# Kernel tuning notes

Hardware: AMD Instinct MI355X
Metric: run time of the kernel (lower is better)

## Reference

```python
import jax, jax.numpy as jnp
import numpy as np
import math

K = 1.0          # Lorentz curvature parameter (points satisfy -t^2 + |s|^2 = -K)
SQRT_K = 1.0
HEADS = 8
HEAD_DIM = 64
EPS_LN = 1e-5


def add_time(xs):
    # lift space vector onto the hyperboloid: t = sqrt(|s|^2 + K)
    t = jnp.sqrt(jnp.sum(xs * xs, axis=-1, keepdims=True) + K)
    return jnp.concatenate([t, xs], axis=-1)


def logmap0(x):
    t, s = x[..., :1], x[..., 1:]
    d = SQRT_K * jnp.arccosh(jnp.maximum(t / SQRT_K, 1.0))
    sn = jnp.maximum(jnp.linalg.norm(s, axis=-1, keepdims=True), 1e-8)
    return jnp.concatenate([jnp.zeros_like(t), d * s / sn], axis=-1)


def expmap0(u):
    s = u[..., 1:]
    n = jnp.maximum(jnp.linalg.norm(s, axis=-1, keepdims=True), 1e-8)
    t = SQRT_K * jnp.cosh(n / SQRT_K)
    return jnp.concatenate([t, SQRT_K * jnp.sinh(n / SQRT_K) * s / n], axis=-1)


def lorentz_ln(x, g, b):
    # LayerNorm on space coords, then recompute time
    s = x[..., 1:]
    mu = jnp.mean(s, axis=-1, keepdims=True)
    var = jnp.var(s, axis=-1, keepdims=True)
    s = (s - mu) / jnp.sqrt(var + EPS_LN) * g + b
    return add_time(s)


def lfc(x, W, activation=None):
    # LorentzFullyConnected: linear on full input -> space coords, recompute time
    s = x @ W.T
    if activation is not None:
        s = activation(s)
    return add_time(s)


def lfc_heads(x, W):
    b, n, _ = x.shape
    s = (x @ W.T).reshape(b, n, HEADS, HEAD_DIM).transpose(0, 2, 1, 3)
    return add_time(s)  # (b, h, n, head_dim+1), per-head time coordinate


def _mha_haa(x, Wq, Wk, Wv, Wo, temperature, beta_raw, tau_raw, lambda_raw):
    q = lfc_heads(x, Wq)
    k = lfc_heads(x, Wk)
    v = lfc_heads(x, Wv)
    q_t, k_t = q[..., :1], k[..., :1]
    q_s, k_s = q[..., 1:], k[..., 1:]
    # Lorentz inner product <q,k>_L = -t_q t_k + <s_q, s_k>, shape (b,h,n,n)
    inner_QK = -q_t @ jnp.swapaxes(k_t, -1, -2) + q_s @ jnp.swapaxes(k_s, -1, -2)
    inner_OQ = -SQRT_K * q_t                       # (b,h,n,1)
    inner_OK = -SQRT_K * jnp.swapaxes(k_t, -1, -2)  # (b,h,1,n)
    norm_sq_QK = jnp.maximum(inner_QK ** 2 / K - K, 0.0)
    norm_sq_OQ = jnp.maximum(inner_OQ ** 2 / K - K, 0.0)
    numer_Z = inner_OK + inner_QK * inner_OQ / K
    denom_Z = jnp.sqrt(norm_sq_QK * norm_sq_OQ + 0.005 ** 2)
    Z = jnp.clip(numer_Z / denom_Z, -1.0, 1.0)
    c_tilde = jnp.arccosh(jnp.maximum(q_t / SQRT_K, 1.0 + 0.001))
    beta = jax.nn.softplus(beta_raw)
    B = jnp.sqrt(jax.nn.relu(1.0 - (beta / jnp.sinh(c_tilde)) ** 2) + 1e-8)
    lam = jax.nn.softplus(lambda_raw)
    dist_raw = SQRT_K * jnp.arccosh(jnp.maximum(-inner_QK / K, 1.0 + 0.001))
    d_soft = 40.0 * jnp.tanh(dist_raw / 40.0)
    sd = d_soft / 15.0
    H = sd + jax.nn.softplus(-2.0 * sd) - math.log(2.0)
    tau = jax.nn.softplus(tau_raw)
    m = 0.1
    Phi = jax.nn.softplus(B + Z - m) - math.log(1.0 + math.exp(-m))
    score = jax.nn.softmax((-lam * H - tau * Phi) / temperature, axis=-1)
    # Lorentz expmap aggregation: weighted mean in tangent space at origin
    v_tan = logmap0(v)
    mean_tan = (score @ v_tan) / (jnp.sum(score, axis=-1, keepdims=True) + 1e-8)
    attn = expmap0(mean_tan).transpose(0, 2, 1, 3)  # (b,n,h,head_dim+1)
    b_, n_ = attn.shape[:2]
    a_s = attn[..., 1:].reshape(b_, n_, -1)   # (b,n,h*head_dim)
    a_t = attn[..., :1].reshape(b_, n_, -1)   # (b,n,h)
    t2 = jnp.sum(a_t ** 2, axis=-1, keepdims=True) - (HEADS - 1) * K
    attn = jnp.concatenate([jnp.sqrt(jnp.maximum(t2, 1e-8)), a_s], axis=-1)
    return lfc(attn, Wo)


def reference(x, Wq, Wk, Wv, Wo, W1, W2, ln1_g, ln1_b, ln2_g, ln2_b,
              temperature, beta_raw, tau_raw, lambda_raw):
    out = _mha_haa(lorentz_ln(x, ln1_g, ln1_b), Wq, Wk, Wv, Wo,
                   temperature, beta_raw, tau_raw, lambda_raw)
    out_s = out[..., 1:] + x[..., 1:]                 # residual on space coords
    y = lorentz_ln(add_time(out_s), ln2_g, ln2_b)
    h = lfc(y, W1, activation=lambda z: jax.nn.gelu(z, approximate=False))
    h = lfc(h, W2)
    out_s = h[..., 1:] + out_s
    return add_time(out_s)


def setup_inputs() -> dict:
    key = jax.random.key(0)
    ks = jax.random.split(key, 8)
    B, N, D = 2, 1024, 513
    xs = 0.5 * jax.random.normal(ks[0], (B, N, D - 1), dtype=jnp.float32)
    x = add_time(xs)
    sc = 1.0 / math.sqrt(D)
    return {
        "x": x,
        "Wq": sc * jax.random.normal(ks[1], (512, 513), dtype=jnp.float32),
        "Wk": sc * jax.random.normal(ks[2], (512, 513), dtype=jnp.float32),
        "Wv": sc * jax.random.normal(ks[3], (512, 513), dtype=jnp.float32),
        "Wo": sc * jax.random.normal(ks[4], (512, 513), dtype=jnp.float32),
        "W1": sc * jax.random.normal(ks[5], (2048, 513), dtype=jnp.float32),
        "W2": (1.0 / math.sqrt(2049)) * jax.random.normal(ks[6], (512, 2049), dtype=jnp.float32),
        "ln1_g": jnp.ones((512,), jnp.float32),
        "ln1_b": jnp.zeros((512,), jnp.float32),
        "ln2_g": jnp.ones((512,), jnp.float32),
        "ln2_b": jnp.zeros((512,), jnp.float32),
        "temperature": jnp.ones((1,), jnp.float32),
        "beta_raw": jnp.full((1,), math.log(math.e - 1.0), jnp.float32),
        "tau_raw": jnp.full((1,), math.log(math.exp(0.1) - 1.0), jnp.float32),
        "lambda_raw": jnp.full((1,), math.log(math.e - 1.0), jnp.float32),
    }
```

## Files before the change

kernel.cpp:

```cpp
#include <hip/hip_runtime.h>
#include <math.h>

#define DEV static __device__ __forceinline__

typedef __bf16 bf16_t;
typedef __bf16 bf16x8 __attribute__((ext_vector_type(8)));
typedef float f32x4 __attribute__((ext_vector_type(4)));

#define MFMA16(a,b,c) __builtin_amdgcn_mfma_f32_16x16x32_bf16(a,b,c,0,0,0)

DEV float frcp(float x){ return __builtin_amdgcn_rcpf(x); }
DEV float softplus_fast(float x){
  return fmaxf(x, 0.f) + __logf(1.f + __expf(-fabsf(x)));
}
DEV float tanh_fast(float z){
  float e2 = __expf(2.f * z);
  return (e2 - 1.f) * frcp(e2 + 1.f);
}
DEV float gelu_fast(float v){
  float u = 0.7978845608028654f * fmaf(0.044715f * v, v * v, v);
  u = fminf(fmaxf(u, -15.f), 15.f);
  return 0.5f * v * (1.f + tanh_fast(u));
}

DEV void gl_lds16(const void* g, void* l) {
  __builtin_amdgcn_global_load_lds((const __attribute__((address_space(1))) void*)g,
                                   (__attribute__((address_space(3))) void*)l, 16, 0, 0);
}

DEV float waveReduceSum(float v){
  #pragma unroll
  for (int o = 32; o > 0; o >>= 1) v += __shfl_xor(v, o, 64);
  return v;
}
DEV float blockReduceSum(float v, float* sh){
  v = waveReduceSum(v);
  int w = threadIdx.x >> 6;
  int nw = blockDim.x >> 6;
  __syncthreads();
  if ((threadIdx.x & 63) == 0) sh[w] = v;
  __syncthreads();
  float r = sh[0];
  for (int i = 1; i < nw; i++) r += sh[i];
  return r;
}

__global__ __launch_bounds__(256) void conv_all(
    const float* __restrict__ Wq, const float* __restrict__ Wk,
    const float* __restrict__ Wv, const float* __restrict__ Wo,
    const float* __restrict__ W1, const float* __restrict__ W2,
    bf16_t* __restrict__ Wqkvb, bf16_t* __restrict__ Wob,
    bf16_t* __restrict__ W1b, bf16_t* __restrict__ W2b,
    float* __restrict__ wqkv0, float* __restrict__ wo0,
    float* __restrict__ w10, float* __restrict__ w20)
{
  long i = (long)blockIdx.x * 256 + threadIdx.x;
  if (i < 786432) {
    long r = i >> 9; int c = (int)(i & 511);
    const float* src = (r < 512) ? Wq + r * 513 : (r < 1024) ? Wk + (r - 512) * 513 : Wv + (r - 1024) * 513;
    Wqkvb[i] = (bf16_t)src[c + 1];
  } else if (i < 1048576) {
    long j = i - 786432;
    long r = j >> 9; int c = (int)(j & 511);
    Wob[j] = (bf16_t)Wo[r * 513 + c + 1];
  } else if (i < 2097152) {
    long j = i - 1048576;
    long r = j >> 9; int c = (int)(j & 511);
    W1b[j] = (bf16_t)W1[r * 513 + c + 1];
  } else if (i < 3145728) {
    long j = i - 2097152;
    long r = j >> 11; int c = (int)(j & 2047);
    W2b[j] = (bf16_t)W2[r * 2049 + c + 1];
  } else if (i < 3150336) {
    int j = (int)(i - 3145728);
    if (j < 1536) {
      wqkv0[j] = (j < 512) ? Wq[(long)j * 513] : (j < 1024) ? Wk[(long)(j - 512) * 513] : Wv[(long)(j - 1024) * 513];
    } else if (j < 2048) wo0[j - 1536] = Wo[(long)(j - 1536) * 513];
    else if (j < 4096)  w10[j - 2048] = W1[(long)(j - 2048) * 513];
    else                w20[j - 4096] = W2[(long)(j - 4096) * 2049];
  }
}

__global__ __launch_bounds__(256) void ln_fwd(
    const float* __restrict__ xin,
    const float* __restrict__ g, const float* __restrict__ b,
    bf16_t* __restrict__ y, float* __restrict__ ty)
{
  __shared__ float sh[8];
  int row = blockIdx.x;
  const float* xr = xin + (long)row * 513 + 1;
  int t = threadIdx.x;
  float a0 = xr[t], a1 = xr[t + 256];
  float s  = blockReduceSum(a0 + a1, sh);
  float s2 = blockReduceSum(a0 * a0 + a1 * a1, sh);
  float mu = s * (1.f / 512.f);
  float var = s2 * (1.f / 512.f) - mu * mu;
  float inv = rsqrtf(var + 1e-5f);
  float y0 = (a0 - mu) * inv * g[t] + b[t];
  float y1v = (a1 - mu) * inv * g[t + 256] + b[t + 256];
  float q = blockReduceSum(y0 * y0 + y1v * y1v, sh);
  bf16_t* yr = y + (long)row * 512;
  yr[t] = (bf16_t)y0;
  yr[t + 256] = (bf16_t)y1v;
  if (t == 0) ty[row] = sqrtf(q + 1.f);
}

__global__ __launch_bounds__(256) void res_ln(
    const float* __restrict__ woA, const float* __restrict__ woB,
    const float* __restrict__ ch2, const float* __restrict__ wo0,
    const float* __restrict__ xin,
    const float* __restrict__ g, const float* __restrict__ b,
    float* __restrict__ outs,
    bf16_t* __restrict__ y, float* __restrict__ ty)
{
  __shared__ float sh[8];
  int row = blockIdx.x;
  int t = threadIdx.x;
  const float* c = ch2 + (long)row * 8;
  float cs = ((c[0] + c[1]) + (c[2] + c[3])) + ((c[4] + c[5]) + (c[6] + c[7]));
  float tattn = sqrtf(fmaxf(cs - 7.f, 1e-8f));
  long i0 = (long)row * 512 + t, i1 = i0 + 256;
  float a0 = woA[i0] + woB[i0] + tattn * wo0[t]       + xin[(long)row * 513 + 1 + t];
  float a1 = woA[i1] + woB[i1] + tattn * wo0[t + 256] + xin[(long)row * 513 + 1 + t + 256];
  outs[i0] = a0;
  outs[i1] = a1;
  float s  = blockReduceSum(a0 + a1, sh);
  float s2 = blockReduceSum(a0 * a0 + a1 * a1, sh);
  float mu = s * (1.f / 512.f);
  float var = s2 * (1.f / 512.f) - mu * mu;
  float inv = rsqrtf(var + 1e-5f);
  float y0 = (a0 - mu) * inv * g[t] + b[t];
  float y1v = (a1 - mu) * inv * g[t + 256] + b[t + 256];
  float q = blockReduceSum(y0 * y0 + y1v * y1v, sh);
  bf16_t* yr = y + (long)row * 512;
  yr[t] = (bf16_t)y0;
  yr[t + 256] = (bf16_t)y1v;
  if (t == 0) ty[row] = sqrtf(q + 1.f);
}

__global__ __launch_bounds__(256) void final_k(
    const float* __restrict__ h2A, const float* __restrict__ h2B,
    const bf16_t* __restrict__ hb, const float* __restrict__ w20,
    const float* __restrict__ outs,
    float* __restrict__ out)
{
  __shared__ float sh[8];
  int row = blockIdx.x;
  int t = threadIdx.x;
  bf16x8 hv = *(const bf16x8*)&hb[(long)row * 2048 + t * 8];
  float ss = 0.f;
  #pragma unroll
  for (int j = 0; j < 8; j++) { float f = (float)hv[j]; ss = fmaf(f, f, ss); }
  float th = sqrtf(blockReduceSum(ss, sh) + 1.f);
  long i0 = (long)row * 512 + t, i1 = i0 + 256;
  float o0 = h2A[i0] + h2B[i0] + th * w20[t]       + outs[i0];
  float o1 = h2A[i1] + h2B[i1] + th * w20[t + 256] + outs[i1];
  float q = blockReduceSum(o0 * o0 + o1 * o1, sh);
  float* yr = out + (long)row * 513;
  yr[1 + t] = o0;
  yr[1 + t + 256] = o1;
  if (t == 0) yr[0] = sqrtf(q + 1.f);
}

__global__ __launch_bounds__(256) void qkv_prep(
    const bf16_t* __restrict__ qkvsb,
    float* __restrict__ qt, float* __restrict__ kt, float* __restrict__ Bi,
    bf16_t* __restrict__ VTt,
    const float* __restrict__ beta_p)
{
  __shared__ bf16_t tile[64 * 72];
  int z = blockIdx.y, b = z >> 3, h = z & 7;
  int n0 = blockIdx.x * 64;
  int t = threadIdx.x;
  int r = t >> 2, c4 = t & 3;
  long rowbase = (long)(b * 1024 + n0 + r) * 1536 + h * 64 + c4 * 16;
  bf16x8 q0 = *(const bf16x8*)(qkvsb + rowbase);
  bf16x8 q1 = *(const bf16x8*)(qkvsb + rowbase + 8);
  bf16x8 k0 = *(const bf16x8*)(qkvsb + rowbase + 512);
  bf16x8 k1 = *(const bf16x8*)(qkvsb + rowbase + 520);
  bf16x8 v0 = *(const bf16x8*)(qkvsb + rowbase + 1024);
  bf16x8 v1 = *(const bf16x8*)(qkvsb + rowbase + 1032);
  float q2 = 0.f, k2 = 0.f, vv2 = 0.f;
  #pragma unroll
  for (int e = 0; e < 8; e++) {
    float a0 = (float)q0[e], a1 = (float)q1[e];
    float b0 = (float)k0[e], b1 = (float)k1[e];
    float c0 = (float)v0[e], c1 = (float)v1[e];
    q2 = fmaf(a0, a0, fmaf(a1, a1, q2));
    k2 = fmaf(b0, b0, fmaf(b1, b1, k2));
    vv2 = fmaf(c0, c0, fmaf(c1, c1, vv2));
  }
  q2 += __shfl_xor(q2, 1, 64); q2 += __shfl_xor(q2, 2, 64);
  k2 += __shfl_xor(k2, 1, 64); k2 += __shfl_xor(k2, 2, 64);
  vv2 += __shfl_xor(vv2, 1, 64); vv2 += __shfl_xor(vv2, 2, 64);
  float vT = sqrtf(1.f + vv2);
  float sn0 = sqrtf(vv2);
  float coef = __logf(vT + sn0) * frcp(fmaxf(sn0, 1e-8f));
  if (c4 == 0) {
    int ob = z * 1024 + n0 + r;
    float qT = sqrtf(1.f + q2);
    qt[ob] = qT;
    kt[ob] = sqrtf(1.f + k2);
    float beta = softplus_fast(beta_p[0]);
    float xq = fmaxf(qT, 1.001f);
    float sh_ = sqrtf(fmaxf(xq * xq - 1.f, 0.f));
    float rr = beta * frcp(sh_);
    Bi[ob] = sqrtf(fmaxf(1.f - rr * rr, 0.f) + 1e-8f);
  }
  #pragma unroll
  for (int e = 0; e < 8; e++) {
    tile[(c4 * 16 + e) * 72 + r]     = (bf16_t)(coef * (float)v0[e]);
    tile[(c4 * 16 + 8 + e) * 72 + r] = (bf16_t)(coef * (float)v1[e]);
  }
  __syncthreads();
  int d = t >> 2, cc = (t & 3) * 16;
  bf16x8 o0 = *(const bf16x8*)&tile[d * 72 + cc];
  bf16x8 o1 = *(const bf16x8*)&tile[d * 72 + cc + 8];
  bf16_t* dst = VTt + (long)z * 64 * 1024 + (long)d * 1024 + n0 + cc;
  *(bf16x8*)dst = o0;
  *(bf16x8*)(dst + 8) = o1;
}

__global__ __launch_bounds__(256) void attn_fused(
    const bf16_t* __restrict__ qkvsb,
    const bf16_t* __restrict__ VTt,
    const float* __restrict__ qt, const float* __restrict__ kt,
    const float* __restrict__ Bi,
    bf16_t* __restrict__ attnb,
    float* __restrict__ ch2,
    const float* __restrict__ lam_p, const float* __restrict__ tau_p,
    const float* __restrict__ temp_p)
{
  __shared__ bf16_t Ks[64 * 64];
  __shared__ bf16_t Vs[64 * 64];
  __shared__ bf16_t Ps[32 * 72];
  __shared__ float ot[32 * 65];
  __shared__ float sh_qt[32], sh_Bc[32], sh_kt[64], rs[32];

  const int t = threadIdx.x;
  const int w = t >> 6;
  const int lane = t & 63;
  const int lm = lane & 15, lh = lane >> 4;
  const int z = blockIdx.y, b = z >> 3, h = z & 7;
  const int n0 = blockIdx.x * 32;
  const int sb = (((lane & 7) ^ (lane >> 3)) << 4);
  const int r8 = lane >> 3;

  float lam = softplus_fast(lam_p[0]);
  float tau = softplus_fast(tau_p[0]);
  float invT = frcp(temp_p[0]);
  float A1 = -lam * invT, A2 = -tau * invT;
  float A2h = 0.5f * A2, K0 = A2 * 0.048750465f;

  if (t < 32) {
    sh_qt[t] = qt[z * 1024 + n0 + t];
    sh_Bc[t] = Bi[z * 1024 + n0 + t] - 0.1f;
    rs[t] = 0.f;
  }

  const bf16_t* qbase = qkvsb + ((long)(b * 1024 + n0) * 1536 + h * 64);
  gl_lds16((const char*)(qbase + (long)(w * 8 + r8) * 1536) + sb, (char*)Ks + w * 1024);
  __syncthreads();
  bf16x8 qf[2][2];
  #pragma unroll
  for (int i = 0; i < 2; i++)
    #pragma unroll
    for (int kk = 0; kk < 2; kk++)
      qf[i][kk] = *(const bf16x8*)&Ks[(i * 16 + lm) * 64 + (((kk * 4 + lh) ^ (lm & 7)) << 3)];

  f32x4 oacc[2] = {};
  float racc[2][4] = {};

  const bf16_t* kbase = qkvsb + ((long)b * 1024 * 1536 + 512 + h * 64);
  const bf16_t* vbase = VTt + (long)z * 64 * 1024;
  const int sl0 = ((lh) ^ (lm & 7)) << 3;
  const int sl1 = ((4 + lh) ^ (lm & 7)) << 3;

  for (int kv = 0; kv < 16; kv++) {
    __syncthreads();
    {
      const bf16_t* kb = kbase + (long)(kv * 64) * 1536;
      gl_lds16((const char*)(kb + (long)(w * 16 + r8) * 1536) + sb,     (char*)Ks + (w * 2) * 1024);
      gl_lds16((const char*)(kb + (long)(w * 16 + 8 + r8) * 1536) + sb, (char*)Ks + (w * 2 + 1) * 1024);
      const bf16_t* vb = vbase + kv * 64;
      gl_lds16((const char*)(vb + (long)(w * 16 + r8) * 1024) + sb,     (char*)Vs + (w * 2) * 1024);
      gl_lds16((const char*)(vb + (long)(w * 16 + 8 + r8) * 1024) + sb, (char*)Vs + (w * 2 + 1) * 1024);
    }
    if (t < 64) sh_kt[t] = kt[z * 1024 + kv * 64 + t];
    __syncthreads();

    f32x4 sacc[2] = {};
    bf16x8 kf0 = *(const bf16x8*)&Ks[(w * 16 + lm) * 64 + sl0];
    bf16x8 kf1 = *(const bf16x8*)&Ks[(w * 16 + lm) * 64 + sl1];
    sacc[0] = MFMA16(qf[0][0], kf0, sacc[0]);
    sacc[0] = MFMA16(qf[0][1], kf1, sacc[0]);
    sacc[1] = MFMA16(qf[1][0], kf0, sacc[1]);
    sacc[1] = MFMA16(qf[1][1], kf1, sacc[1]);

    float ktv = sh_kt[w * 16 + lm];
    #pragma unroll
    for (int i = 0; i < 2; i++) {
      #pragma unroll
      for (int q = 0; q < 4; q++) {
        int r = i * 16 + lh * 4 + q;
        float qtv = sh_qt[r], Bc = sh_Bc[r];
        float nOQ = fmaf(qtv, qtv, -1.f);
        float inner = fmaf(-qtv, ktv, sacc[i][q]);
        float nQK = fmaxf(fmaf(inner, inner, -1.f), 0.f);
        float ri = __builtin_amdgcn_rsqf(fmaf(nQK, nOQ, 2.5e-5f));
        float zr = fmaf(inner, qtv, ktv) * ri;
        float Zc = fminf(fmaxf(-zr, -1.f), 1.f);
        float xx = fmaxf(-inner, 1.001f);
        float u = fmaf(__log2f(xx), 0.01732868f, 0.01732868f);
        float p = fminf(u * u, 0.09f);
        float H = p * fmaf(p, -6.584f, 3.5556f);
        float a = Zc + Bc;
        float a2 = a * a;
        float lc = a2 * fmaf(a2, fmaf(a2, 0.00034722f, -0.0052083f), 0.125f);
        float lgt = fmaf(A1, H, fmaf(A2, lc, fmaf(A2h, a, K0)));
        float e = __expf(lgt);
        Ps[r * 72 + w * 16 + lm] = (bf16_t)e;
        racc[i][q] += e;
      }
    }
    __syncthreads();

    bf16x8 va0 = *(const bf16x8*)&Vs[(w * 16 + lm) * 64 + sl0];
    bf16x8 va1 = *(const bf16x8*)&Vs[(w * 16 + lm) * 64 + sl1];
    bf16x8 pb00 = *(const bf16x8*)&Ps[lm * 72 + lh * 8];
    bf16x8 pb01 = *(const bf16x8*)&Ps[lm * 72 + 32 + lh * 8];
    bf16x8 pb10 = *(const bf16x8*)&Ps[(16 + lm) * 72 + lh * 8];
    bf16x8 pb11 = *(const bf16x8*)&Ps[(16 + lm) * 72 + 32 + lh * 8];
    oacc[0] = MFMA16(va0, pb00, oacc[0]);
    oacc[0] = MFMA16(va1, pb01, oacc[0]);
    oacc[1] = MFMA16(va0, pb10, oacc[1]);
    oacc[1] = MFMA16(va1, pb11, oacc[1]);
  }

  #pragma unroll
  for (int i = 0; i < 2; i++)
    #pragma unroll
    for (int q = 0; q < 4; q++) {
      float v = racc[i][q];
      v += __shfl_xor(v, 1, 64);
      v += __shfl_xor(v, 2, 64);
      v += __shfl_xor(v, 4, 64);
      v += __shfl_xor(v, 8, 64);
      if (lm == 0) atomicAdd(&rs[i * 16 + lh * 4 + q], v);
    }

  #pragma unroll
  for (int j = 0; j < 2; j++)
    #pragma unroll
    for (int q = 0; q < 4; q++)
      ot[(j * 16 + lm) * 65 + w * 16 + lh * 4 + q] = oacc[j][q];
  __syncthreads();

  int r = t >> 3, c0 = (t & 7) * 8;
  float inv = frcp(rs[r] * (1.f + 1e-8f));
  float v[8];
  float ss = 0.f;
  #pragma unroll
  for (int e = 0; e < 8; e++) {
    v[e] = ot[r * 65 + c0 + e] * inv;
    ss = fmaf(v[e], v[e], ss);
  }
  ss += __shfl_xor(ss, 1, 64);
  ss += __shfl_xor(ss, 2, 64);
  ss += __shfl_xor(ss, 4, 64);
  float nn = fmaxf(sqrtf(ss), 1e-8f);
  float e_ = __expf(nn), ei = frcp(e_);
  float coef = 0.5f * (e_ - ei) * frcp(nn);
  bf16x8 ov;
  #pragma unroll
  for (int e = 0; e < 8; e++) ov[e] = (bf16_t)(coef * v[e]);
  *(bf16x8*)(attnb + (long)(b * 1024 + n0 + r) * 512 + h * 64 + c0) = ov;
  if (c0 == 0) {
    float ch = 0.5f * (e_ + ei);
    ch2[(long)(b * 1024 + n0 + r) * 8 + h] = ch * ch;
  }
}

template<int ACTF>
DEV void gemm_rep_body(
    const bf16_t* __restrict__ Ag, int lda,
    const bf16_t* __restrict__ Bg, int ldb,
    bf16_t* __restrict__ Cg, int ldc, int K,
    const float* __restrict__ trow, const float* __restrict__ w0)
{
  __shared__ char smem[24576];
  __shared__ float sh_t[128];
  bf16_t* As = (bf16_t*)smem;
  bf16_t* Bs = (bf16_t*)(smem + 16384);
  const int t = threadIdx.x;
  const int wid = t >> 6, lane = t & 63;
  const int lm = lane & 15, lh = lane >> 4;
  const int bm = blockIdx.x * 128;
  const int bn = blockIdx.y * 64;
  const int wm = (wid >> 1) * 64;
  const int wn = (wid & 1) * 32;
  const int sb = (((lane & 7) ^ (lane >> 3)) << 4);
  const int r8 = lane >> 3;
  f32x4 acc[4][2] = {};

  if (t < 128) sh_t[t] = trow[bm + t];
  float w0c[2] = { w0[bn + wn + lm], w0[bn + wn + 16 + lm] };

  for (int kk = 0; kk < K; kk += 64) {
    __syncthreads();
    #pragma unroll
    for (int r = 0; r < 4; r++) {
      int chunk = wid * 4 + r;
      gl_lds16((const char*)(Ag + (long)(bm + chunk * 8 + r8) * lda + kk) + sb,
               smem + chunk * 1024);
    }
    #pragma unroll
    for (int r = 0; r < 2; r++) {
      int chunk = wid * 2 + r;
      gl_lds16((const char*)(Bg + (long)(bn + chunk * 8 + r8) * ldb + kk) + sb,
               smem + 16384 + chunk * 1024);
    }
    __syncthreads();
    #pragma unroll
    for (int k2 = 0; k2 < 2; k2++) {
      const int sl = (((k2 * 4 + lh) ^ (lm & 7)) << 3);
      bf16x8 af[4], bfr[2];
      #pragma unroll
      for (int i = 0; i < 4; i++) af[i] = *(const bf16x8*)&As[(wm + i * 16 + lm) * 64 + sl];
      #pragma unroll
      for (int j = 0; j < 2; j++) bfr[j] = *(const bf16x8*)&Bs[(wn + j * 16 + lm) * 64 + sl];
      #pragma unroll
      for (int i = 0; i < 4; i++)
        #pragma unroll
        for (int j = 0; j < 2; j++)
          acc[i][j] = MFMA16(af[i], bfr[j], acc[i][j]);
    }
  }

  __syncthreads();
  bf16_t* rep = (bf16_t*)smem;
  #pragma unroll
  for (int i = 0; i < 4; i++) {
    #pragma unroll
    for (int q = 0; q < 4; q++) {
      int r = wm + i * 16 + lh * 4 + q;
      #pragma unroll
      for (int j = 0; j < 2; j++) {
        float v = acc[i][j][q] + sh_t[r] * w0c[j];
        rep[r * 64 + wn + j * 16 + lm] = (bf16_t)(ACTF == 0 ? gelu_fast(v) : v);
      }
    }
  }
  __syncthreads();

  #pragma unroll
  for (int rd = 0; rd < 4; rd++) {
    int off = rd * 4096 + t * 16;
    int lr = off >> 7;
    int lc = (off & 127) >> 1;
    bf16x8 vv = *(const bf16x8*)(smem + off);
    *(bf16x8*)(Cg + (long)(bm + lr) * ldc + bn + lc) = vv;
  }
}

DEV void gemm_f32_body(
    const bf16_t* __restrict__ Ag, int lda,
    const bf16_t* __restrict__ Bg, int ldb,
    float* __restrict__ Cg, int ldc,
    int k0, int k1)
{
  __shared__ bf16_t As[64 * 64];
  __shared__ bf16_t Bs[64 * 64];
  const int t = threadIdx.x;
  const int wid = t >> 6, lane = t & 63;
  const int lm = lane & 15, lh = lane >> 4;
  const int bm = blockIdx.x * 64;
  const int bn = blockIdx.y * 64;
  const int wm = (wid >> 1) * 32;
  const int wn = (wid & 1) * 32;
  const int sb = (((lane & 7) ^ (lane >> 3)) << 4);
  const int r8 = lane >> 3;
  f32x4 acc[2][2] = {};

  for (int kk = k0; kk < k1; kk += 64) {
    __syncthreads();
    #pragma unroll
    for (int r = 0; r < 2; r++) {
      int chunk = wid * 2 + r;
      gl_lds16((const char*)(Ag + (long)(bm + chunk * 8 + r8) * lda + kk) + sb,
               (char*)As + chunk * 1024);
      gl_lds16((const char*)(Bg + (long)(bn + chunk * 8 + r8) * ldb + kk) + sb,
               (char*)Bs + chunk * 1024);
    }
    __syncthreads();
    #pragma unroll
    for (int k2 = 0; k2 < 2; k2++) {
      const int sl = (((k2 * 4 + lh) ^ (lm & 7)) << 3);
      bf16x8 af[2], bfr[2];
      #pragma unroll
      for (int i = 0; i < 2; i++) af[i] = *(const bf16x8*)&As[(wm + i * 16 + lm) * 64 + sl];
      #pragma unroll
      for (int j = 0; j < 2; j++) bfr[j] = *(const bf16x8*)&Bs[(wn + j * 16 + lm) * 64 + sl];
      #pragma unroll
      for (int i = 0; i < 2; i++)
        #pragma unroll
        for (int j = 0; j < 2; j++)
          acc[i][j] = MFMA16(af[i], bfr[j], acc[i][j]);
    }
  }

  #pragma unroll
  for (int i = 0; i < 2; i++) {
    #pragma unroll
    for (int q = 0; q < 4; q++) {
      long row = bm + wm + i * 16 + lh * 4 + q;
      #pragma unroll
      for (int j = 0; j < 2; j++)
        Cg[row * ldc + bn + wn + j * 16 + lm] = acc[i][j][q];
    }
  }
}

__global__ __launch_bounds__(256) void gemm_qkv(const bf16_t* A, int lda, const bf16_t* B, int ldb,
                                                bf16_t* C, int ldc, int K,
                                                const float* trow, const float* w0){
  gemm_rep_body<2>(A, lda, B, ldb, C, ldc, K, trow, w0);
}
__global__ __launch_bounds__(256) void gemm_f1(const bf16_t* A, int lda, const bf16_t* B, int ldb,
                                               bf16_t* C, int ldc, int K,
                                               const float* trow, const float* w0){
  gemm_rep_body<0>(A, lda, B, ldb, C, ldc, K, trow, w0);
}
__global__ __launch_bounds__(256) void gemm_wo(const bf16_t* A, int lda, const bf16_t* B, int ldb,
                                               float* C, int ldc, int K, int kcut){
  int k0 = blockIdx.z ? kcut : 0;
  int k1 = blockIdx.z ? K : kcut;
  gemm_f32_body(A, lda, B, ldb, C + (long)blockIdx.z * 2048 * ldc, ldc, k0, k1);
}
__global__ __launch_bounds__(256) void gemm_f2(const bf16_t* A, int lda, const bf16_t* B, int ldb,
                                               float* C, int ldc, int K, int kcut){
  int k0 = blockIdx.z ? kcut : 0;
  int k1 = blockIdx.z ? K : kcut;
  gemm_f32_body(A, lda, B, ldb, C + (long)blockIdx.z * 2048 * ldc, ldc, k0, k1);
}

extern "C" void kernel_launch(void* const* d_in, const int* in_sizes, int n_in,
                              void* d_out, int out_size, void* d_ws, size_t ws_size,
                              hipStream_t stream) {
  const float* x    = (const float*)d_in[0];
  const float* Wq   = (const float*)d_in[1];
  const float* Wk   = (const float*)d_in[2];
  const float* Wv   = (const float*)d_in[3];
  const float* Wo   = (const float*)d_in[4];
  const float* W1   = (const float*)d_in[5];
  const float* W2   = (const float*)d_in[6];
  const float* g1   = (const float*)d_in[7];
  const float* b1   = (const float*)d_in[8];
  const float* g2   = (const float*)d_in[9];
  const float* b2   = (const float*)d_in[10];
  const float* temp = (const float*)d_in[11];
  const float* beta = (const float*)d_in[12];
  const float* tau  = (const float*)d_in[13];
  const float* lam  = (const float*)d_in[14];

  char* W = (char*)d_ws;
  bf16_t* Wqkvb = (bf16_t*)(W + 0);
  bf16_t* Wob   = (bf16_t*)(W + 1572864);
  bf16_t* W1b   = (bf16_t*)(W + 2097152);
  bf16_t* W2b   = (bf16_t*)(W + 4194304);
  float*  wqkv0 = (float*) (W + 6291456);
  float*  wo0   = (float*) (W + 6297600);
  float*  w10   = (float*) (W + 6299648);
  float*  w20   = (float*) (W + 6307840);
  bf16_t* y1b   = (bf16_t*)(W + 6309888);
  float*  ty1   = (float*) (W + 8407040);
  bf16_t* qkvsb = (bf16_t*)(W + 8415232);
  float*  qt    = (float*) (W + 14706688);
  float*  kt    = (float*) (W + 14772224);
  float*  Bi    = (float*) (W + 14837760);
  bf16_t* VTt   = (bf16_t*)(W + 14903296);
  float*  ch2   = (float*) (W + 17000448);
  bf16_t* attnb = (bf16_t*)(W + 17065984);
  float*  tmpA  = (float*) (W + 19163136);
  float*  tmpB  = (float*) (W + 23357440);
  float*  outs  = (float*) (W + 27551744);
  bf16_t* y2b   = (bf16_t*)(W + 31746048);
  float*  ty2   = (float*) (W + 33843200);
  bf16_t* hb    = (bf16_t*)(W + 33851392);

  conv_all<<<12306, 256, 0, stream>>>(Wq, Wk, Wv, Wo, W1, W2,
                                      Wqkvb, Wob, W1b, W2b, wqkv0, wo0, w10, w20);

  ln_fwd<<<2048, 256, 0, stream>>>(x, g1, b1, y1b, ty1);

  gemm_qkv<<<dim3(16,24,1),256,0,stream>>>(y1b, 512, Wqkvb, 512, qkvsb, 1536, 512, ty1, wqkv0);

  qkv_prep<<<dim3(16,16,1),256,0,stream>>>(qkvsb, qt, kt, Bi, VTt, beta);

  attn_fused<<<dim3(32,16,1),256,0,stream>>>(qkvsb, VTt, qt, kt, Bi, attnb, ch2, lam, tau, temp);

  gemm_wo<<<dim3(32,8,2),256,0,stream>>>(attnb, 512, Wob, 512, tmpA, 512, 512, 256);

  res_ln<<<2048, 256, 0, stream>>>(tmpA, tmpB, ch2, wo0, x, g2, b2, outs, y2b, ty2);

  gemm_f1<<<dim3(16,32,1),256,0,stream>>>(y2b, 512, W1b, 512, hb, 2048, 512, ty2, w10);

  gemm_f2<<<dim3(32,8,2),256,0,stream>>>(hb, 2048, W2b, 2048, tmpA, 512, 2048, 1024);

  final_k<<<2048, 256, 0, stream>>>(tmpA, tmpB, hb, w20, outs, (float*)d_out);
}
```

Before: 102.0 us.

## Fuse LN into weight prep, move norm stats into GEMM epilogues, swizzle XCDs

Several changes land together. The first LayerNorm is merged into the weight-conversion kernel, saving one launch. The q/k time coordinates and Bi, plus the per-tile hidden norm partials, are now computed in the QKV and FFN1 GEMM epilogues, so the later kernels no longer re-read q/k or the full hidden tensor. Block indices are swizzled across XCDs in the attention and GEMM kernels, and FFN2 is split four ways along K instead of two. The costs are extra epilogue work in the GEMMs, more fp32 partial buffers to sum in final_k, and a different summation order for the split-K partials.

```diff
diff --git a/kernel.cpp b/kernel.cpp
--- a/kernel.cpp
+++ b/kernel.cpp
@@ -45,16 +45,47 @@
   return r;
 }
 
-__global__ __launch_bounds__(256) void conv_all(
+DEV int2 xcd_swz(int gx, int gy){
+  int id = blockIdx.y * gx + blockIdx.x;
+  int q = (gx * gy) >> 3;
+  int s = (id & 7) * q + (id >> 3);
+  int2 r; r.x = s % gx; r.y = s / gx;
+  return r;
+}
+
+__global__ __launch_bounds__(256) void prep(
+    const float* __restrict__ xin,
+    const float* __restrict__ g, const float* __restrict__ b,
     const float* __restrict__ Wq, const float* __restrict__ Wk,
     const float* __restrict__ Wv, const float* __restrict__ Wo,
     const float* __restrict__ W1, const float* __restrict__ W2,
+    bf16_t* __restrict__ y, float* __restrict__ ty,
     bf16_t* __restrict__ Wqkvb, bf16_t* __restrict__ Wob,
     bf16_t* __restrict__ W1b, bf16_t* __restrict__ W2b,
     float* __restrict__ wqkv0, float* __restrict__ wo0,
     float* __restrict__ w10, float* __restrict__ w20)
 {
-  long i = (long)blockIdx.x * 256 + threadIdx.x;
+  int t = threadIdx.x;
+  if (blockIdx.x < 2048) {
+    __shared__ float sh[8];
+    int row = blockIdx.x;
+    const float* xr = xin + (long)row * 513 + 1;
+    float a0 = xr[t], a1 = xr[t + 256];
+    float s  = blockReduceSum(a0 + a1, sh);
+    float s2 = blockReduceSum(a0 * a0 + a1 * a1, sh);
+    float mu = s * (1.f / 512.f);
+    float var = s2 * (1.f / 512.f) - mu * mu;
+    float inv = rsqrtf(var + 1e-5f);
+    float y0 = (a0 - mu) * inv * g[t] + b[t];
+    float y1v = (a1 - mu) * inv * g[t + 256] + b[t + 256];
+    float q = blockReduceSum(y0 * y0 + y1v * y1v, sh);
+    bf16_t* yr = y + (long)row * 512;
+    yr[t] = (bf16_t)y0;
+    yr[t + 256] = (bf16_t)y1v;
+    if (t == 0) ty[row] = sqrtf(q + 1.f);
+    return;
+  }
+  long i = (long)(blockIdx.x - 2048) * 256 + t;
   if (i < 786432) {
     long r = i >> 9; int c = (int)(i & 511);
     const float* src = (r < 512) ? Wq + r * 513 : (r < 1024) ? Wk + (r - 512) * 513 : Wv + (r - 1024) * 513;
@@ -79,30 +110,6 @@
     else if (j < 4096)  w10[j - 2048] = W1[(long)(j - 2048) * 513];
     else                w20[j - 4096] = W2[(long)(j - 4096) * 2049];
   }
-}
-
-__global__ __launch_bounds__(256) void ln_fwd(
-    const float* __restrict__ xin,
-    const float* __restrict__ g, const float* __restrict__ b,
-    bf16_t* __restrict__ y, float* __restrict__ ty)
-{
-  __shared__ float sh[8];
-  int row = blockIdx.x;
-  const float* xr = xin + (long)row * 513 + 1;
-  int t = threadIdx.x;
-  float a0 = xr[t], a1 = xr[t + 256];
-  float s  = blockReduceSum(a0 + a1, sh);
-  float s2 = blockReduceSum(a0 * a0 + a1 * a1, sh);
-  float mu = s * (1.f / 512.f);
-  float var = s2 * (1.f / 512.f) - mu * mu;
-  float inv = rsqrtf(var + 1e-5f);
-  float y0 = (a0 - mu) * inv * g[t] + b[t];
-  float y1v = (a1 - mu) * inv * g[t + 256] + b[t + 256];
-  float q = blockReduceSum(y0 * y0 + y1v * y1v, sh);
-  bf16_t* yr = y + (long)row * 512;
-  yr[t] = (bf16_t)y0;
-  yr[t + 256] = (bf16_t)y1v;
-  if (t == 0) ty[row] = sqrtf(q + 1.f);
 }
 
 __global__ __launch_bounds__(256) void res_ln(
@@ -139,22 +146,21 @@
 }
 
 __global__ __launch_bounds__(256) void final_k(
-    const float* __restrict__ h2A, const float* __restrict__ h2B,
-    const bf16_t* __restrict__ hb, const float* __restrict__ w20,
+    const float* __restrict__ hA, const float* __restrict__ hB,
+    const float* __restrict__ hC, const float* __restrict__ hD,
+    const float* __restrict__ th2p, const float* __restrict__ w20,
     const float* __restrict__ outs,
     float* __restrict__ out)
 {
   __shared__ float sh[8];
   int row = blockIdx.x;
   int t = threadIdx.x;
-  bf16x8 hv = *(const bf16x8*)&hb[(long)row * 2048 + t * 8];
-  float ss = 0.f;
-  #pragma unroll
-  for (int j = 0; j < 8; j++) { float f = (float)hv[j]; ss = fmaf(f, f, ss); }
-  float th = sqrtf(blockReduceSum(ss, sh) + 1.f);
+  float p = (t < 32) ? th2p[(long)t * 2048 + row] : 0.f;
+  float hn = blockReduceSum(p, sh);
+  float th = sqrtf(hn + 1.f);
   long i0 = (long)row * 512 + t, i1 = i0 + 256;
-  float o0 = h2A[i0] + h2B[i0] + th * w20[t]       + outs[i0];
-  float o1 = h2A[i1] + h2B[i1] + th * w20[t + 256] + outs[i1];
+  float o0 = (hA[i0] + hB[i0]) + (hC[i0] + hD[i0]) + th * w20[t]       + outs[i0];
+  float o1 = (hA[i1] + hB[i1]) + (hC[i1] + hD[i1]) + th * w20[t + 256] + outs[i1];
   float q = blockReduceSum(o0 * o0 + o1 * o1, sh);
   float* yr = out + (long)row * 513;
   yr[1 + t] = o0;
@@ -162,51 +168,28 @@
   if (t == 0) yr[0] = sqrtf(q + 1.f);
 }
 
-__global__ __launch_bounds__(256) void qkv_prep(
-    const bf16_t* __restrict__ qkvsb,
-    float* __restrict__ qt, float* __restrict__ kt, float* __restrict__ Bi,
-    bf16_t* __restrict__ VTt,
-    const float* __restrict__ beta_p)
+__global__ __launch_bounds__(256) void vtan_tr(
+    const bf16_t* __restrict__ qkvsb, bf16_t* __restrict__ VTt)
 {
   __shared__ bf16_t tile[64 * 72];
   int z = blockIdx.y, b = z >> 3, h = z & 7;
   int n0 = blockIdx.x * 64;
   int t = threadIdx.x;
   int r = t >> 2, c4 = t & 3;
-  long rowbase = (long)(b * 1024 + n0 + r) * 1536 + h * 64 + c4 * 16;
-  bf16x8 q0 = *(const bf16x8*)(qkvsb + rowbase);
-  bf16x8 q1 = *(const bf16x8*)(qkvsb + rowbase + 8);
-  bf16x8 k0 = *(const bf16x8*)(qkvsb + rowbase + 512);
-  bf16x8 k1 = *(const bf16x8*)(qkvsb + rowbase + 520);
-  bf16x8 v0 = *(const bf16x8*)(qkvsb + rowbase + 1024);
-  bf16x8 v1 = *(const bf16x8*)(qkvsb + rowbase + 1032);
-  float q2 = 0.f, k2 = 0.f, vv2 = 0.f;
+  const bf16_t* vb = qkvsb + ((long)(b * 1024 + n0 + r) * 1536 + 1024 + h * 64 + c4 * 16);
+  bf16x8 v0 = *(const bf16x8*)vb;
+  bf16x8 v1 = *(const bf16x8*)(vb + 8);
+  float ss = 0.f;
   #pragma unroll
   for (int e = 0; e < 8; e++) {
-    float a0 = (float)q0[e], a1 = (float)q1[e];
-    float b0 = (float)k0[e], b1 = (float)k1[e];
-    float c0 = (float)v0[e], c1 = (float)v1[e];
-    q2 = fmaf(a0, a0, fmaf(a1, a1, q2));
-    k2 = fmaf(b0, b0, fmaf(b1, b1, k2));
-    vv2 = fmaf(c0, c0, fmaf(c1, c1, vv2));
-  }
-  q2 += __shfl_xor(q2, 1, 64); q2 += __shfl_xor(q2, 2, 64);
-  k2 += __shfl_xor(k2, 1, 64); k2 += __shfl_xor(k2, 2, 64);
-  vv2 += __shfl_xor(vv2, 1, 64); vv2 += __shfl_xor(vv2, 2, 64);
-  float vT = sqrtf(1.f + vv2);
-  float sn0 = sqrtf(vv2);
+    float f0 = (float)v0[e], f1 = (float)v1[e];
+    ss = fmaf(f0, f0, fmaf(f1, f1, ss));
+  }
+  ss += __shfl_xor(ss, 1, 64);
+  ss += __shfl_xor(ss, 2, 64);
+  float vT = sqrtf(1.f + ss);
+  float sn0 = sqrtf(ss);
   float coef = __logf(vT + sn0) * frcp(fmaxf(sn0, 1e-8f));
-  if (c4 == 0) {
-    int ob = z * 1024 + n0 + r;
-    float qT = sqrtf(1.f + q2);
-    qt[ob] = qT;
-    kt[ob] = sqrtf(1.f + k2);
-    float beta = softplus_fast(beta_p[0]);
-    float xq = fmaxf(qT, 1.001f);
-    float sh_ = sqrtf(fmaxf(xq * xq - 1.f, 0.f));
-    float rr = beta * frcp(sh_);
-    Bi[ob] = sqrtf(fmaxf(1.f - rr * rr, 0.f) + 1e-8f);
-  }
   #pragma unroll
   for (int e = 0; e < 8; e++) {
     tile[(c4 * 16 + e) * 72 + r]     = (bf16_t)(coef * (float)v0[e]);
@@ -241,8 +224,9 @@
   const int w = t >> 6;
   const int lane = t & 63;
   const int lm = lane & 15, lh = lane >> 4;
-  const int z = blockIdx.y, b = z >> 3, h = z & 7;
-  const int n0 = blockIdx.x * 32;
+  int2 sw = xcd_swz(32, 16);
+  const int z = sw.y, b = z >> 3, h = z & 7;
+  const int n0 = sw.x * 32;
   const int sb = (((lane & 7) ^ (lane >> 3)) << 4);
   const int r8 = lane >> 3;
 
@@ -381,12 +365,15 @@
   }
 }
 
-template<int ACTF>
+template<int ACTF, int STATS>
 DEV void gemm_rep_body(
     const bf16_t* __restrict__ Ag, int lda,
     const bf16_t* __restrict__ Bg, int ldb,
     bf16_t* __restrict__ Cg, int ldc, int K,
-    const float* __restrict__ trow, const float* __restrict__ w0)
+    const float* __restrict__ trow, const float* __restrict__ w0,
+    float* __restrict__ s0, float* __restrict__ s1, float* __restrict__ s2,
+    const float* __restrict__ beta_p,
+    int bx, int by)
 {
   __shared__ char smem[24576];
   __shared__ float sh_t[128];
@@ -395,8 +382,8 @@
   const int t = threadIdx.x;
   const int wid = t >> 6, lane = t & 63;
   const int lm = lane & 15, lh = lane >> 4;
-  const int bm = blockIdx.x * 128;
-  const int bn = blockIdx.y * 64;
+  const int bm = bx * 128;
+  const int bn = by * 64;
   const int wm = (wid >> 1) * 64;
   const int wn = (wid & 1) * 32;
   const int sb = (((lane & 7) ^ (lane >> 3)) << 4);
@@ -461,21 +448,57 @@
     bf16x8 vv = *(const bf16x8*)(smem + off);
     *(bf16x8*)(Cg + (long)(bm + lr) * ldc + bn + lc) = vv;
   }
+
+  if constexpr (STATS != 0) {
+    int rr = t >> 1, half = t & 1;
+    const bf16_t* rp = rep + rr * 64 + half * 32;
+    float s = 0.f;
+    #pragma unroll
+    for (int c = 0; c < 4; c++) {
+      bf16x8 vv = *(const bf16x8*)(rp + c * 8);
+      #pragma unroll
+      for (int e = 0; e < 8; e++) { float f = (float)vv[e]; s = fmaf(f, f, s); }
+    }
+    s += __shfl_xor(s, 1, 64);
+    if (half == 0) {
+      if constexpr (STATS == 2) {
+        s0[(long)(bn >> 6) * 2048 + bm + rr] = s;
+      } else {
+        int bnh = bn >> 6;
+        if (bnh < 16) {
+          int grow = bm + rr, bloc = grow >> 10, n = grow & 1023;
+          if (bnh < 8) {
+            int zz = bloc * 8 + bnh;
+            float qT = sqrtf(1.f + s);
+            s0[zz * 1024 + n] = qT;
+            float beta = softplus_fast(beta_p[0]);
+            float xq = fmaxf(qT, 1.001f);
+            float sh_ = sqrtf(fmaxf(xq * xq - 1.f, 0.f));
+            float rr0 = beta * frcp(sh_);
+            s2[zz * 1024 + n] = sqrtf(fmaxf(1.f - rr0 * rr0, 0.f) + 1e-8f);
+          } else {
+            int zz = bloc * 8 + (bnh - 8);
+            s1[zz * 1024 + n] = sqrtf(1.f + s);
+          }
+        }
+      }
+    }
+  }
 }
 
 DEV void gemm_f32_body(
     const bf16_t* __restrict__ Ag, int lda,
     const bf16_t* __restrict__ Bg, int ldb,
     float* __restrict__ Cg, int ldc,
-    int k0, int k1)
+    int k0, int k1, int bx, int by)
 {
   __shared__ bf16_t As[64 * 64];
   __shared__ bf16_t Bs[64 * 64];
   const int t = threadIdx.x;
   const int wid = t >> 6, lane = t & 63;
   const int lm = lane & 15, lh = lane >> 4;
-  const int bm = blockIdx.x * 64;
-  const int bn = blockIdx.y * 64;
+  const int bm = bx * 64;
+  const int bn = by * 64;
   const int wm = (wid >> 1) * 32;
   const int wn = (wid & 1) * 32;
   const int sb = (((lane & 7) ^ (lane >> 3)) << 4);
@@ -523,25 +546,31 @@
 
 __global__ __launch_bounds__(256) void gemm_qkv(const bf16_t* A, int lda, const bf16_t* B, int ldb,
                                                 bf16_t* C, int ldc, int K,
-                                                const float* trow, const float* w0){
-  gemm_rep_body<2>(A, lda, B, ldb, C, ldc, K, trow, w0);
+                                                const float* trow, const float* w0,
+                                                float* qt, float* kt, float* Bi, const float* beta){
+  int2 sw = xcd_swz(16, 24);
+  gemm_rep_body<2, 1>(A, lda, B, ldb, C, ldc, K, trow, w0, qt, kt, Bi, beta, sw.x, sw.y);
 }
 __global__ __launch_bounds__(256) void gemm_f1(const bf16_t* A, int lda, const bf16_t* B, int ldb,
                                                bf16_t* C, int ldc, int K,
-                                               const float* trow, const float* w0){
-  gemm_rep_body<0>(A, lda, B, ldb, C, ldc, K, trow, w0);
+                                               const float* trow, const float* w0,
+                                               float* th2p){
+  int2 sw = xcd_swz(16, 32);
+  gemm_rep_body<0, 2>(A, lda, B, ldb, C, ldc, K, trow, w0, th2p, nullptr, nullptr, nullptr, sw.x, sw.y);
 }
 __global__ __launch_bounds__(256) void gemm_wo(const bf16_t* A, int lda, const bf16_t* B, int ldb,
-                                               float* C, int ldc, int K, int kcut){
-  int k0 = blockIdx.z ? kcut : 0;
-  int k1 = blockIdx.z ? K : kcut;
-  gemm_f32_body(A, lda, B, ldb, C + (long)blockIdx.z * 2048 * ldc, ldc, k0, k1);
+                                               float* C, int ldc, int K){
+  int2 sw = xcd_swz(32, 8);
+  int k0 = blockIdx.z * (K >> 1);
+  gemm_f32_body(A, lda, B, ldb, C + (long)blockIdx.z * 2048 * ldc, ldc,
+                k0, k0 + (K >> 1), sw.x, sw.y);
 }
 __global__ __launch_bounds__(256) void gemm_f2(const bf16_t* A, int lda, const bf16_t* B, int ldb,
-                                               float* C, int ldc, int K, int kcut){
-  int k0 = blockIdx.z ? kcut : 0;
-  int k1 = blockIdx.z ? K : kcut;
-  gemm_f32_body(A, lda, B, ldb, C + (long)blockIdx.z * 2048 * ldc, ldc, k0, k1);
+                                               float* C, int ldc, int K){
+  int2 sw = xcd_swz(32, 8);
+  int k0 = blockIdx.z * (K >> 2);
+  gemm_f32_body(A, lda, B, ldb, C + (long)blockIdx.z * 2048 * ldc, ldc,
+                k0, k0 + (K >> 2), sw.x, sw.y);
 }
 
 extern "C" void kernel_launch(void* const* d_in, const int* in_sizes, int n_in,
@@ -582,30 +611,32 @@
   float*  ch2   = (float*) (W + 17000448);
   bf16_t* attnb = (bf16_t*)(W + 17065984);
   float*  tmpA  = (float*) (W + 19163136);
-  float*  tmpB  = (float*) (W + 23357440);
-  float*  outs  = (float*) (W + 27551744);
-  bf16_t* y2b   = (bf16_t*)(W + 31746048);
-  float*  ty2   = (float*) (W + 33843200);
-  bf16_t* hb    = (bf16_t*)(W + 33851392);
-
-  conv_all<<<12306, 256, 0, stream>>>(Wq, Wk, Wv, Wo, W1, W2,
-                                      Wqkvb, Wob, W1b, W2b, wqkv0, wo0, w10, w20);
-
-  ln_fwd<<<2048, 256, 0, stream>>>(x, g1, b1, y1b, ty1);
-
-  gemm_qkv<<<dim3(16,24,1),256,0,stream>>>(y1b, 512, Wqkvb, 512, qkvsb, 1536, 512, ty1, wqkv0);
-
-  qkv_prep<<<dim3(16,16,1),256,0,stream>>>(qkvsb, qt, kt, Bi, VTt, beta);
+  float*  outs  = (float*) (W + 35940352);
+  bf16_t* y2b   = (bf16_t*)(W + 40134656);
+  float*  ty2   = (float*) (W + 42231808);
+  bf16_t* hb    = (bf16_t*)(W + 42240000);
+  float*  th2p  = (float*) (W + 50628608);
+  float*  tmpB  = tmpA + 1048576;
+  float*  tmpC  = tmpA + 2097152;
+  float*  tmpD  = tmpA + 3145728;
+
+  prep<<<14354, 256, 0, stream>>>(x, g1, b1, Wq, Wk, Wv, Wo, W1, W2,
+                                  y1b, ty1, Wqkvb, Wob, W1b, W2b, wqkv0, wo0, w10, w20);
+
+  gemm_qkv<<<dim3(16,24,1),256,0,stream>>>(y1b, 512, Wqkvb, 512, qkvsb, 1536, 512,
+                                           ty1, wqkv0, qt, kt, Bi, beta);
+
+  vtan_tr<<<dim3(16,16,1),256,0,stream>>>(qkvsb, VTt);
 
   attn_fused<<<dim3(32,16,1),256,0,stream>>>(qkvsb, VTt, qt, kt, Bi, attnb, ch2, lam, tau, temp);
 
-  gemm_wo<<<dim3(32,8,2),256,0,stream>>>(attnb, 512, Wob, 512, tmpA, 512, 512, 256);
+  gemm_wo<<<dim3(32,8,2),256,0,stream>>>(attnb, 512, Wob, 512, tmpA, 512, 512);
 
   res_ln<<<2048, 256, 0, stream>>>(tmpA, tmpB, ch2, wo0, x, g2, b2, outs, y2b, ty2);
 
-  gemm_f1<<<dim3(16,32,1),256,0,stream>>>(y2b, 512, W1b, 512, hb, 2048, 512, ty2, w10);
-
-  gemm_f2<<<dim3(32,8,2),256,0,stream>>>(hb, 2048, W2b, 2048, tmpA, 512, 2048, 1024);
-
-  final_k<<<2048, 256, 0, stream>>>(tmpA, tmpB, hb, w20, outs, (float*)d_out);
-}
+  gemm_f1<<<dim3(16,32,1),256,0,stream>>>(y2b, 512, W1b, 512, hb, 2048, 512, ty2, w10, th2p);
+
+  gemm_f2<<<dim3(32,8,4),256,0,stream>>>(hb, 2048, W2b, 2048, tmpA, 512, 2048);
+
+  final_k<<<2048, 256, 0, stream>>>(tmpA, tmpB, tmpC, tmpD, th2p, w20, outs, (float*)d_out);
+}
```

After: 101.7 us. Within noise of the previous version (-0.3%).
